# Optimization experiments

Measured on AMD Instinct MI355X. Metric: run time of the kernel, lower is better.

Reference implementation:

```python
import jax, jax.numpy as jnp
import numpy as np

B, T, H, W, C = 1, 16, 56, 56, 256
NH = 8
WS = (8, 7, 7)
SS = (4, 3, 3)
HID = 4 * C
N = WS[0] * WS[1] * WS[2]  # 392 tokens per window


def _rel_index(ws):
    wt, wh, ww = ws
    coords = np.stack(np.meshgrid(np.arange(wt), np.arange(wh), np.arange(ww), indexing='ij'))
    cf = coords.reshape(3, -1)
    rel = (cf[:, :, None] - cf[:, None, :]).transpose(1, 2, 0)
    rel[..., 0] += wt - 1
    rel[..., 1] += wh - 1
    rel[..., 2] += ww - 1
    rel[..., 0] *= (2 * wh - 1) * (2 * ww - 1)
    rel[..., 1] *= 2 * ww - 1
    return rel.sum(-1)  # (N, N) int


def _win_part_np(x, ws):
    b, t, h, w, c = x.shape
    x = x.reshape(b, t // ws[0], ws[0], h // ws[1], ws[1], w // ws[2], ws[2], c)
    return x.transpose(0, 1, 3, 5, 2, 4, 6, 7).reshape(-1, ws[0] * ws[1] * ws[2], c)


def _attn_mask(t, h, w, ws, ss):
    # static numpy construction of the shifted-window mask (nW, N, N)
    img = np.zeros((1, t, h, w, 1), dtype=np.float32)
    cnt = 0
    for d in (slice(-ws[0]), slice(-ws[0], -ss[0]), slice(-ss[0], None)):
        for hh in (slice(-ws[1]), slice(-ws[1], -ss[1]), slice(-ss[1], None)):
            for ww_ in (slice(-ws[2]), slice(-ws[2], -ss[2]), slice(-ss[2], None)):
                img[:, d, hh, ww_, :] = cnt
                cnt += 1
    mw = _win_part_np(img, ws).squeeze(-1)  # (nW, N)
    diff = mw[:, None, :] - mw[:, :, None]
    return np.where(diff != 0, np.float32(-100.0), np.float32(0.0))


_RPI = jnp.asarray(_rel_index(WS).reshape(-1))
_MASK = jnp.asarray(_attn_mask(T, H, W, WS, SS))  # (nW, N, N)


def _ln(x, g, b, eps=1e-5):
    mu = x.mean(-1, keepdims=True)
    var = ((x - mu) ** 2).mean(-1, keepdims=True)
    return (x - mu) * jax.lax.rsqrt(var + eps) * g + b


def _win_part(x, ws):
    b, t, h, w, c = x.shape
    x = x.reshape(b, t // ws[0], ws[0], h // ws[1], ws[1], w // ws[2], ws[2], c)
    return x.transpose(0, 1, 3, 5, 2, 4, 6, 7).reshape(-1, ws[0] * ws[1] * ws[2], c)


def _win_rev(win, ws, t, h, w):
    b = win.shape[0] // (t * h * w // (ws[0] * ws[1] * ws[2]))
    x = win.reshape(b, t // ws[0], h // ws[1], w // ws[2], ws[0], ws[1], ws[2], -1)
    return x.transpose(0, 1, 4, 2, 5, 3, 6, 7).reshape(b, t, h, w, -1)


def setup_inputs() -> dict:
    key = jax.random.key(0)
    ks = jax.random.split(key, 16)
    n_bias = (2 * WS[0] - 1) * (2 * WS[1] - 1) * (2 * WS[2] - 1)
    return {
        'x': jax.random.normal(ks[0], (B, T, H, W, C), jnp.float32),
        'norm1_g': jnp.ones((C,), jnp.float32),
        'norm1_b': jnp.zeros((C,), jnp.float32),
        'qkv_w': 0.02 * jax.random.normal(ks[1], (3 * C, C), jnp.float32),
        'qkv_b': jnp.zeros((3 * C,), jnp.float32),
        'rpb_table': 0.02 * jax.random.normal(ks[2], (n_bias, NH), jnp.float32),
        'proj_w': 0.02 * jax.random.normal(ks[3], (C, C), jnp.float32),
        'proj_b': jnp.zeros((C,), jnp.float32),
        'norm2_g': jnp.ones((C,), jnp.float32),
        'norm2_b': jnp.zeros((C,), jnp.float32),
        'fc1_w': 0.02 * jax.random.normal(ks[4], (HID, C), jnp.float32),
        'fc1_b': jnp.zeros((HID,), jnp.float32),
        'fc2_w': 0.02 * jax.random.normal(ks[5], (C, HID), jnp.float32),
        'fc2_b': jnp.zeros((C,), jnp.float32),
    }


def reference(x, norm1_g, norm1_b, qkv_w, qkv_b, rpb_table, proj_w, proj_b,
              norm2_g, norm2_b, fc1_w, fc1_b, fc2_w, fc2_b):
    hd = C // NH
    scale = hd ** -0.5
    shortcut = x
    h1 = _ln(x, norm1_g, norm1_b)
    # cyclic shift
    h1 = jnp.roll(h1, (-SS[0], -SS[1], -SS[2]), axis=(1, 2, 3))
    xw = _win_part(h1, WS)  # (B_, N, C)
    B_ = xw.shape[0]
    qkv = xw @ qkv_w.T + qkv_b  # (B_, N, 3C)
    qkv = qkv.reshape(B_, N, 3, NH, hd).transpose(2, 0, 3, 1, 4)
    q, k, v = qkv[0], qkv[1], qkv[2]  # (B_, NH, N, hd)
    attn = jnp.einsum('bhnd,bhmd->bhnm', q * scale, k)
    bias = rpb_table[_RPI].reshape(N, N, NH).transpose(2, 0, 1)  # (NH, N, N)
    attn = attn + bias[None]
    nW = _MASK.shape[0]
    attn = attn.reshape(B_ // nW, nW, NH, N, N) + _MASK[None, :, None]
    attn = jax.nn.softmax(attn, axis=-1).reshape(B_, NH, N, N)
    out = jnp.einsum('bhnm,bhmd->bhnd', attn, v).transpose(0, 2, 1, 3).reshape(B_, N, C)
    out = out @ proj_w.T + proj_b
    out = _win_rev(out, WS, T, H, W)
    out = jnp.roll(out, (SS[0], SS[1], SS[2]), axis=(1, 2, 3))
    x = shortcut + out
    # MLP with residual
    h2 = _ln(x, norm2_g, norm2_b)
    h2 = jax.nn.gelu(h2 @ fc1_w.T + fc1_b, approximate=False)
    return x + (h2 @ fc2_w.T + fc2_b)
```

## Files before the change

kernel.cpp:

```cpp
#include <hip/hip_runtime.h>
#include <hip/hip_bf16.h>
#include <cmath>

typedef unsigned short u16;
typedef unsigned int u32;

using bf16x8 = __attribute__((ext_vector_type(8))) short;
using f32x4  = __attribute__((ext_vector_type(4))) float;

__device__ __forceinline__ float b2f(u16 u) {
  union { u32 i; float f; } x; x.i = ((u32)u) << 16; return x.f;
}
__device__ __forceinline__ u16 f2b(float f) {
  union { float f; u32 i; } x; x.f = f;
  u32 r = x.i + 0x7fffu + ((x.i >> 16) & 1u);
  return (u16)(r >> 16);
}
__device__ __forceinline__ u32 cvtpk(float lo, float hi) {
  u32 r;
  asm("v_cvt_pk_bf16_f32 %0, %1, %2" : "=v"(r) : "v"(lo), "v"(hi));
  return r;
}
__device__ __forceinline__ float vexp2(float x) {
  float r;
  asm("v_exp_f32 %0, %1" : "=v"(r) : "v"(x));
  return r;
}
__device__ __forceinline__ void gload_lds16(const u16* g, u16* l) {
  __builtin_amdgcn_global_load_lds(
      (const __attribute__((address_space(1))) unsigned int*)g,
      (__attribute__((address_space(3))) unsigned int*)l, 16, 0, 0);
}

__global__ __launch_bounds__(256) void pre_k(
    const float* __restrict__ x, const float* __restrict__ n1g,
    const float* __restrict__ n1b, const float* __restrict__ qkvw,
    const float* __restrict__ projw, const float* __restrict__ fc1w,
    const float* __restrict__ fc2w, const float* __restrict__ rpb,
    u16* __restrict__ xw, u16* __restrict__ wts, u16* __restrict__ biasB) {
  const int blk = blockIdx.x;
  const int tid = threadIdx.x;
  if (blk < 12544) {
    const int wid = tid >> 6, lane = tid & 63;
    const int row = blk * 4 + wid;
    int widx = row / 392, n = row - widx * 392;
    int wt = widx >> 6, wh = (widx >> 3) & 7, ww = widx & 7;
    int ti = n / 49, rem = n - ti * 49, hi = rem / 7, wi = rem - hi * 7;
    int t = (wt * 8 + ti + 4) & 15;
    int h = wh * 7 + hi + 3; if (h >= 56) h -= 56;
    int w = ww * 7 + wi + 3; if (w >= 56) w -= 56;
    int srow = (t * 56 + h) * 56 + w;
    float4 v = *(const float4*)(x + (size_t)srow * 256 + lane * 4);
    float s = v.x + v.y + v.z + v.w;
    float sq = v.x * v.x + v.y * v.y + v.z * v.z + v.w * v.w;
    for (int o = 1; o < 64; o <<= 1) {
      s += __shfl_xor(s, o, 64);
      sq += __shfl_xor(sq, o, 64);
    }
    float mu = s * (1.0f / 256.0f);
    float rstd = rsqrtf(sq * (1.0f / 256.0f) - mu * mu + 1e-5f);
    float4 gg = *(const float4*)(n1g + lane * 4);
    float4 bb = *(const float4*)(n1b + lane * 4);
    ushort4 ov;
    ov.x = f2b((v.x - mu) * rstd * gg.x + bb.x);
    ov.y = f2b((v.y - mu) * rstd * gg.y + bb.y);
    ov.z = f2b((v.z - mu) * rstd * gg.z + bb.z);
    ov.w = f2b((v.w - mu) * rstd * gg.w + bb.w);
    *(ushort4*)(xw + (size_t)row * 256 + lane * 4) = ov;
  } else if (blk < 14144) {
    const int b = blk - 12544;
    const int sl = b / 25, qt = b - sl * 25;
    const int head = sl & 7, cls = sl >> 3;
    const int tb = (cls >> 2) & 1, hb = (cls >> 1) & 1, wb = cls & 1;
    const int lm = tid >> 4, kl = tid & 15;
    int q = qt * 16 + lm; if (q > 391) q = 391;
    const int ti = q / 49, rem = q - ti * 49, hi = rem / 7, wi = rem - hi * 7;
    const int cq = ti * 169 + hi * 13 + wi;
    const int rtq = tb ? (ti < 4 ? 1 : 2) : 0;
    const int rhq = hb ? (hi < 4 ? 1 : 2) : 0;
    const int rwq = wb ? (wi < 4 ? 1 : 2) : 0;
    const int labq = rtq * 9 + rhq * 3 + rwq;
    u16* ob = biasB + (size_t)b * 6400 + tid;
    for (int t = 0; t < 25; t++) {
      int k = t * 16 + kl;
      float v;
      if (k < 392) {
        int tk = k / 49, rk = k - tk * 49, hk = rk / 7, wk = rk - hk * 7;
        int ck = tk * 169 + hk * 13 + wk;
        float bv = rpb[(cq - ck + 1267) * 8 + head];
        int rt = tb ? (tk < 4 ? 1 : 2) : 0;
        int rh = hb ? (hk < 4 ? 1 : 2) : 0;
        int rw = wb ? (wk < 4 ? 1 : 2) : 0;
        if (rt * 9 + rh * 3 + rw != labq) bv -= 100.f;
        v = bv * 1.4426950408889634f;
      } else {
        v = -2081.f;
      }
      ob[t * 256] = f2b(v);
    }
  } else {
    int i = (blk - 14144) * 256 + tid;
    const float* src;
    int off;
    if (i < 196608)      { src = qkvw;  off = 0; }
    else if (i < 262144) { src = projw; off = 196608; }
    else if (i < 524288) { src = fc1w;  off = 262144; }
    else                 { src = fc2w;  off = 524288; }
    wts[i] = f2b(src[i - off]);
  }
}

__global__ __launch_bounds__(256) void ln_k(const float* __restrict__ src,
                                            const float* __restrict__ g,
                                            const float* __restrict__ b,
                                            u16* __restrict__ dst) {
  const int wid = threadIdx.x >> 6, lane = threadIdx.x & 63;
  const int row = blockIdx.x * 4 + wid;
  float4 v = *(const float4*)(src + (size_t)row * 256 + lane * 4);
  float s = v.x + v.y + v.z + v.w;
  float sq = v.x * v.x + v.y * v.y + v.z * v.z + v.w * v.w;
  for (int o = 1; o < 64; o <<= 1) {
    s += __shfl_xor(s, o, 64);
    sq += __shfl_xor(sq, o, 64);
  }
  float mu = s * (1.0f / 256.0f);
  float rstd = rsqrtf(sq * (1.0f / 256.0f) - mu * mu + 1e-5f);
  float4 gg = *(const float4*)(g + lane * 4);
  float4 bb = *(const float4*)(b + lane * 4);
  ushort4 ov;
  ov.x = f2b((v.x - mu) * rstd * gg.x + bb.x);
  ov.y = f2b((v.y - mu) * rstd * gg.y + bb.y);
  ov.z = f2b((v.z - mu) * rstd * gg.z + bb.z);
  ov.w = f2b((v.w - mu) * rstd * gg.w + bb.w);
  *(ushort4*)(dst + (size_t)row * 256 + lane * 4) = ov;
}

template <int EPI>
__global__ __launch_bounds__(512) void gemm_k(const u16* __restrict__ A,
                                              const u16* __restrict__ Bw,
                                              int K, int tilesN,
                                              const float* __restrict__ bias,
                                              u16* __restrict__ outb,
                                              float* __restrict__ outf,
                                              const float* __restrict__ res,
                                              float qscale) {
  __shared__ __align__(16) u16 As[2][256 * 32];
  __shared__ __align__(16) u16 Bs[2][128 * 32];
  const int tid = threadIdx.x;
  const int swzb = ((int)blockIdx.x & 7) * ((int)gridDim.x >> 3) +
                   ((int)blockIdx.x >> 3);
  const int tm = swzb / tilesN, tn = swzb - tm * tilesN;
  const int wid = tid >> 6, lane = tid & 63;
  const int wm = wid >> 1, wn = wid & 1;
  const int lm = lane & 15, lk = lane >> 4;
  f32x4 acc[4][4] = {};
  const u16* Ap = A + (size_t)tm * 256 * K;
  const u16* Bp = Bw + (size_t)tn * 128 * K;

  const int sA0 = wid * 128;
  const int sB0 = wid * 64;
  const int nt = K >> 5;

#define STAGE(bufi, kk)                                                       \
  {                                                                           \
    int S = sA0 + lane, r = S >> 2, cs = S & 3;                               \
    gload_lds16(Ap + (size_t)r * K + (kk) + ((cs ^ ((r >> 1) & 3)) << 3),     \
                &As[bufi][sA0 * 8]);                                          \
    S = sA0 + 64 + lane; r = S >> 2; cs = S & 3;                              \
    gload_lds16(Ap + (size_t)r * K + (kk) + ((cs ^ ((r >> 1) & 3)) << 3),     \
                &As[bufi][(sA0 + 64) * 8]);                                   \
    S = sB0 + lane; r = S >> 2; cs = S & 3;                                   \
    gload_lds16(Bp + (size_t)r * K + (kk) + ((cs ^ ((r >> 1) & 3)) << 3),     \
                &Bs[bufi][sB0 * 8]);                                          \
  }

  STAGE(0, 0);
  for (int t = 0; t < nt; t++) {
    const int cur = t & 1;
    if (t + 1 < nt) {
      STAGE(cur ^ 1, (t + 1) << 5);
      asm volatile("s_waitcnt vmcnt(3)" ::: "memory");
    } else {
      asm volatile("s_waitcnt vmcnt(0)" ::: "memory");
    }
    asm volatile("s_barrier" ::: "memory");
    __builtin_amdgcn_sched_barrier(0);
    bf16x8 af[4], bfr[4];
#pragma unroll
    for (int f = 0; f < 4; f++) {
      int ra = wm * 64 + f * 16 + lm;
      int rb = wn * 64 + f * 16 + lm;
      af[f] = *(const bf16x8*)((const char*)&As[cur][0] + ra * 64 +
                               ((lk ^ ((ra >> 1) & 3)) << 4));
      bfr[f] = *(const bf16x8*)((const char*)&Bs[cur][0] + rb * 64 +
                                ((lk ^ ((rb >> 1) & 3)) << 4));
    }
#pragma unroll
    for (int fm = 0; fm < 4; fm++)
#pragma unroll
      for (int fn = 0; fn < 4; fn++)
        acc[fm][fn] = __builtin_amdgcn_mfma_f32_16x16x32_bf16(
            af[fm], bfr[fn], acc[fm][fn], 0, 0, 0);
    asm volatile("s_barrier" ::: "memory");
  }
#undef STAGE

  const int rbase = tm * 256 + wm * 64, cbase = tn * 128 + wn * 64;
#pragma unroll
  for (int fm = 0; fm < 4; fm++) {
#pragma unroll
    for (int fn = 0; fn < 4; fn++) {
      const int col = cbase + fn * 16 + lm;
#pragma unroll
      for (int r = 0; r < 4; r++) {
        const int row = rbase + fm * 16 + lk * 4 + r;
        float v = acc[fm][fn][r] + bias[col];
        if (EPI == 0) {
          int s = col >> 8, rem = col & 255, head = rem >> 5, d = rem & 31;
          int widx = row / 392, n = row - widx * 392;
          size_t o;
          if (s == 2) {
            int c = n >> 5, gg2 = (n >> 3) & 3, e = n & 7;
            int lm2 = d & 15, half = d >> 4;
            o = 25690112u + (size_t)(widx * 8 + head) * 13312 +
                (size_t)(((c * 2 + half) * 64) + gg2 * 16 + lm2) * 8 + e;
          } else {
            if (s == 0) v *= qscale;
            o = (size_t)s * 12845056u +
                (((size_t)(widx * 8 + head)) * 392 + n) * 32 + d;
          }
          outb[o] = f2b(v);
        } else if (EPI == 1) {
          int widx = row / 392, n = row - widx * 392;
          int wt = widx >> 6, wh = (widx >> 3) & 7, ww = widx & 7;
          int ti = n / 49, rem2 = n - ti * 49, hi = rem2 / 7, wi = rem2 - hi * 7;
          int t = (wt * 8 + ti + 4) & 15;
          int h = wh * 7 + hi + 3; if (h >= 56) h -= 56;
          int w = ww * 7 + wi + 3; if (w >= 56) w -= 56;
          size_t dr = ((size_t)(t * 56 + h)) * 56 + w;
          outf[dr * 256 + col] = res[dr * 256 + col] + v;
        } else if (EPI == 2) {
          float gv = 0.5f * v * (1.0f + erff(v * 0.70710678f));
          outb[(size_t)row * 1024 + col] = f2b(gv);
        } else {
          outf[(size_t)row * 256 + col] = res[(size_t)row * 256 + col] + v;
        }
      }
    }
  }
}

__global__ __launch_bounds__(256) void attn_k(const u16* __restrict__ qg,
                                              const u16* __restrict__ kg,
                                              const u16* __restrict__ vfg,
                                              const u16* __restrict__ biasB,
                                              u16* __restrict__ attno) {
  __shared__ __align__(16) char lds[59904];
  const int bid = blockIdx.x;
  const int widx = bid >> 3;
  const int tid = threadIdx.x;
  const size_t base = (size_t)bid * 12544;
  const int tb = (widx >> 6) & 1;
  const int hb = (((widx >> 3) & 7) == 7) ? 1 : 0;
  const int wb = ((widx & 7) == 7) ? 1 : 0;
  const int sl = (tb * 4 + hb * 2 + wb) * 8 + (bid & 7);
  const int VOFF = 25088;
  const int POFF = 51712;

#pragma unroll
  for (int i = 0; i < 6; i++) {
    int s = i * 256 + tid, r = s >> 2, cs = s & 3;
    gload_lds16(kg + base + r * 32 + ((cs ^ ((r >> 1) & 3)) << 3),
                (u16*)(lds + (size_t)(i * 256 + (tid & ~63)) * 16));
  }
  if (tid < 32) {
    int s = 1536 + tid, r = s >> 2, cs = s & 3;
    gload_lds16(kg + base + r * 32 + ((cs ^ ((r >> 1) & 3)) << 3),
                (u16*)(lds + (size_t)1536 * 16));
  }
  {
    const u16* vsrc = vfg + (size_t)bid * 13312;
#pragma unroll
    for (int i = 0; i < 6; i++) {
      int s = i * 256 + tid;
      gload_lds16(vsrc + (size_t)s * 8,
                  (u16*)(lds + VOFF + (size_t)(i * 256 + (tid & ~63)) * 16));
    }
    if (tid < 128) {
      int s = 1536 + tid;
      gload_lds16(vsrc + (size_t)s * 8,
                  (u16*)(lds + VOFF + (size_t)(1536 + (tid & ~63)) * 16));
    }
  }
  __syncthreads();

  const int w = tid >> 6, lane = tid & 63;
  const int g = lane >> 4, lm = lane & 15;
  const int kswz = ((lm >> 1) & 3);
  char* PqW = lds + POFF + w * 2048 + lm * 128;
  const int swz = (lm & 7) << 4;
  const char* vlds = lds + VOFF + lane * 16;

  for (int qt = w; qt < 25; qt += 4) {
    const int q = qt * 16 + lm;
    const int qr = q < 391 ? q : 391;
    bf16x8 qf = *(const bf16x8*)(qg + base + (size_t)qr * 32 + g * 8);
    const u16* bp = biasB + ((size_t)(sl * 25 + qt) * 25) * 256 + lm * 16 + 4 * g;
    f32x4 st[25];
#pragma unroll
    for (int t = 0; t < 25; t++) {
      ushort4 bb = *(const ushort4*)(bp + t * 256);
      f32x4 bacc = {b2f(bb.x), b2f(bb.y), b2f(bb.z), b2f(bb.w)};
      int kr = (t < 24) ? (16 * t + lm) : (384 + (lm & 7));
      bf16x8 kf = *(const bf16x8*)(lds + kr * 64 + ((g ^ kswz) << 4));
      st[t] = __builtin_amdgcn_mfma_f32_16x16x32_bf16(kf, qf, bacc, 0, 0, 0);
    }
    float m = -3e38f;
#pragma unroll
    for (int t = 0; t < 25; t++)
      m = fmaxf(m, fmaxf(fmaxf(st[t][0], st[t][1]), fmaxf(st[t][2], st[t][3])));
    m = fmaxf(m, __shfl_xor(m, 16, 64));
    m = fmaxf(m, __shfl_xor(m, 32, 64));

    float sum = 0.f;
    f32x4 oa0 = {0.f, 0.f, 0.f, 0.f}, oa1 = {0.f, 0.f, 0.f, 0.f};
#pragma unroll
    for (int c = 0; c < 13; c++) {
      const int p64 = (c & 1) << 6;
      {
        int t = 2 * c;
        float e0 = vexp2(st[t][0] - m), e1 = vexp2(st[t][1] - m);
        float e2 = vexp2(st[t][2] - m), e3 = vexp2(st[t][3] - m);
        sum += (e0 + e1) + (e2 + e3);
        uint2 pp;
        pp.x = cvtpk(e0, e1);
        pp.y = cvtpk(e2, e3);
        *(uint2*)(PqW + ((p64 + 8 * g) ^ swz)) = pp;
      }
      {
        uint2 pp;
        if (c < 12) {
          int t = 2 * c + 1;
          float e0 = vexp2(st[t][0] - m), e1 = vexp2(st[t][1] - m);
          float e2 = vexp2(st[t][2] - m), e3 = vexp2(st[t][3] - m);
          sum += (e0 + e1) + (e2 + e3);
          pp.x = cvtpk(e0, e1);
          pp.y = cvtpk(e2, e3);
        } else {
          pp.x = 0u; pp.y = 0u;
        }
        *(uint2*)(PqW + ((p64 + 32 + 8 * g) ^ swz)) = pp;
      }
      bf16x8 pf = *(const bf16x8*)(PqW + ((p64 + 16 * g) ^ swz));
      const char* vp = vlds + c * 2048;
      bf16x8 v0 = *(const bf16x8*)vp;
      bf16x8 v1 = *(const bf16x8*)(vp + 1024);
      oa0 = __builtin_amdgcn_mfma_f32_16x16x32_bf16(pf, v0, oa0, 0, 0, 0);
      oa1 = __builtin_amdgcn_mfma_f32_16x16x32_bf16(pf, v1, oa1, 0, 0, 0);
    }
    sum += __shfl_xor(sum, 16, 64);
    sum += __shfl_xor(sum, 32, 64);
    const float inv = 1.f / sum;
#pragma unroll
    for (int r = 0; r < 4; r++) {
      int qq = qt * 16 + 4 * g + r;
      if (qq < 392) {
        u16* op = attno + ((size_t)(widx * 392 + qq)) * 256 + (bid & 7) * 32;
        op[lm] = f2b(oa0[r] * inv);
        op[16 + lm] = f2b(oa1[r] * inv);
      }
    }
  }
}

extern "C" void kernel_launch(void* const* d_in, const int* in_sizes, int n_in,
                              void* d_out, int out_size, void* d_ws,
                              size_t ws_size, hipStream_t stream) {
  const float* x     = (const float*)d_in[0];
  const float* n1g   = (const float*)d_in[1];
  const float* n1b   = (const float*)d_in[2];
  const float* qkvw  = (const float*)d_in[3];
  const float* qkvb  = (const float*)d_in[4];
  const float* rpb   = (const float*)d_in[5];
  const float* projw = (const float*)d_in[6];
  const float* projb = (const float*)d_in[7];
  const float* n2g   = (const float*)d_in[8];
  const float* n2b   = (const float*)d_in[9];
  const float* fc1w  = (const float*)d_in[10];
  const float* fc1b  = (const float*)d_in[11];
  const float* fc2w  = (const float*)d_in[12];
  const float* fc2b  = (const float*)d_in[13];

  const size_t NEED = 130547712;
  if (ws_size < NEED) return;

  char* ws = (char*)d_ws;
  u16* xw      = (u16*)(ws + 0LL);
  u16* qb      = (u16*)(ws + 25690112LL);
  u16* attno   = (u16*)(ws + 0LL);
  u16* h2      = (u16*)(ws + 0LL);
  u16* hid     = (u16*)(ws + 25690112LL);
  u16* biasB   = (u16*)(ws + 104333312LL);
  u16* wq      = (u16*)(ws + 128974848LL);
  u16* wp      = (u16*)(ws + 129368064LL);
  u16* w1      = (u16*)(ws + 129499136LL);
  u16* w2      = (u16*)(ws + 130023424LL);
  float* xres  = (float*)d_out;

  pre_k<<<17216, 256, 0, stream>>>(x, n1g, n1b, qkvw, projw, fc1w, fc2w, rpb,
                                   xw, wq, biasB);
  gemm_k<0><<<196 * 6, 512, 0, stream>>>(
      xw, wq, 256, 6, qkvb, qb, nullptr, nullptr,
      0.17677669529663687f * 1.4426950408889634f);
  attn_k<<<1024, 256, 0, stream>>>(qb, qb + 12845056, qb + 2 * 12845056, biasB,
                                   attno);
  gemm_k<1><<<196 * 2, 512, 0, stream>>>(attno, wp, 256, 2, projb, nullptr,
                                         xres, x, 0.f);
  ln_k<<<12544, 256, 0, stream>>>(xres, n2g, n2b, h2);
  gemm_k<2><<<196 * 8, 512, 0, stream>>>(h2, w1, 256, 8, fc1b, hid, nullptr,
                                         nullptr, 0.f);
  gemm_k<3><<<196 * 2, 512, 0, stream>>>(hid, w2, 1024, 2, fc2b, nullptr,
                                         (float*)d_out, xres, 0.f);
}
```

Baseline: 291.9 us.

## Fuse projection GEMM with residual and LayerNorm; use polynomial erf GELU

```diff
diff --git a/kernel.cpp b/kernel.cpp
--- a/kernel.cpp
+++ b/kernel.cpp
@@ -30,6 +30,18 @@
   __builtin_amdgcn_global_load_lds(
       (const __attribute__((address_space(1))) unsigned int*)g,
       (__attribute__((address_space(3))) unsigned int*)l, 16, 0, 0);
+}
+__device__ __forceinline__ float fast_gelu(float v) {
+  float u = 0.70710678118f * v;
+  float au = fabsf(u);
+  float t = 1.f / (1.f + 0.3275911f * au);
+  float p = t * (0.254829592f +
+            t * (-0.284496736f +
+            t * (1.421413741f + t * (-1.453152027f + t * 1.061405429f))));
+  float e = vexp2(-au * au * 1.4426950408889634f);
+  float erf_abs = 1.f - p * e;
+  float er = (v < 0.f) ? -erf_abs : erf_abs;
+  return 0.5f * v * (1.f + er);
 }
 
 __global__ __launch_bounds__(256) void pre_k(
@@ -110,31 +122,6 @@
   }
 }
 
-__global__ __launch_bounds__(256) void ln_k(const float* __restrict__ src,
-                                            const float* __restrict__ g,
-                                            const float* __restrict__ b,
-                                            u16* __restrict__ dst) {
-  const int wid = threadIdx.x >> 6, lane = threadIdx.x & 63;
-  const int row = blockIdx.x * 4 + wid;
-  float4 v = *(const float4*)(src + (size_t)row * 256 + lane * 4);
-  float s = v.x + v.y + v.z + v.w;
-  float sq = v.x * v.x + v.y * v.y + v.z * v.z + v.w * v.w;
-  for (int o = 1; o < 64; o <<= 1) {
-    s += __shfl_xor(s, o, 64);
-    sq += __shfl_xor(sq, o, 64);
-  }
-  float mu = s * (1.0f / 256.0f);
-  float rstd = rsqrtf(sq * (1.0f / 256.0f) - mu * mu + 1e-5f);
-  float4 gg = *(const float4*)(g + lane * 4);
-  float4 bb = *(const float4*)(b + lane * 4);
-  ushort4 ov;
-  ov.x = f2b((v.x - mu) * rstd * gg.x + bb.x);
-  ov.y = f2b((v.y - mu) * rstd * gg.y + bb.y);
-  ov.z = f2b((v.z - mu) * rstd * gg.z + bb.z);
-  ov.w = f2b((v.w - mu) * rstd * gg.w + bb.w);
-  *(ushort4*)(dst + (size_t)row * 256 + lane * 4) = ov;
-}
-
 template <int EPI>
 __global__ __launch_bounds__(512) void gemm_k(const u16* __restrict__ A,
                                               const u16* __restrict__ Bw,
@@ -230,23 +217,153 @@
                 (((size_t)(widx * 8 + head)) * 392 + n) * 32 + d;
           }
           outb[o] = f2b(v);
-        } else if (EPI == 1) {
-          int widx = row / 392, n = row - widx * 392;
-          int wt = widx >> 6, wh = (widx >> 3) & 7, ww = widx & 7;
-          int ti = n / 49, rem2 = n - ti * 49, hi = rem2 / 7, wi = rem2 - hi * 7;
-          int t = (wt * 8 + ti + 4) & 15;
-          int h = wh * 7 + hi + 3; if (h >= 56) h -= 56;
-          int w = ww * 7 + wi + 3; if (w >= 56) w -= 56;
-          size_t dr = ((size_t)(t * 56 + h)) * 56 + w;
-          outf[dr * 256 + col] = res[dr * 256 + col] + v;
         } else if (EPI == 2) {
-          float gv = 0.5f * v * (1.0f + erff(v * 0.70710678f));
-          outb[(size_t)row * 1024 + col] = f2b(gv);
+          outb[(size_t)row * 1024 + col] = f2b(fast_gelu(v));
         } else {
           outf[(size_t)row * 256 + col] = res[(size_t)row * 256 + col] + v;
         }
       }
     }
+  }
+}
+
+__global__ __launch_bounds__(512) void proj_ln_k(
+    const u16* __restrict__ A, const u16* __restrict__ Bw,
+    const float* __restrict__ pb, const float* __restrict__ x,
+    const float* __restrict__ n2g, const float* __restrict__ n2b,
+    float* __restrict__ xres, u16* __restrict__ h2) {
+  __shared__ __align__(16) u16 As[2][128 * 32];
+  __shared__ __align__(16) u16 Bs[2][256 * 32];
+  const int tid = threadIdx.x;
+  const int tm = ((int)blockIdx.x & 7) * ((int)gridDim.x >> 3) +
+                 ((int)blockIdx.x >> 3);
+  const int wid = tid >> 6, lane = tid & 63;
+  const int wm = wid >> 2, wn = wid & 3;
+  const int lm = lane & 15, lk = lane >> 4;
+  f32x4 acc[4][4] = {};
+  const u16* Ap = A + (size_t)tm * 128 * 256;
+
+#define PSTAGE(bufi, kk)                                                      \
+  {                                                                           \
+    int S = wid * 64 + lane, r = S >> 2, cs = S & 3;                          \
+    gload_lds16(A + (size_t)tm * 32768 + (size_t)r * 256 + (kk) +             \
+                    ((cs ^ ((r >> 1) & 3)) << 3),                             \
+                &As[bufi][(wid * 64) * 8]);                                   \
+    S = wid * 128 + lane; r = S >> 2; cs = S & 3;                             \
+    gload_lds16(Bw + (size_t)r * 256 + (kk) + ((cs ^ ((r >> 1) & 3)) << 3),   \
+                &Bs[bufi][(wid * 128) * 8]);                                  \
+    S = wid * 128 + 64 + lane; r = S >> 2; cs = S & 3;                        \
+    gload_lds16(Bw + (size_t)r * 256 + (kk) + ((cs ^ ((r >> 1) & 3)) << 3),   \
+                &Bs[bufi][(wid * 128 + 64) * 8]);                             \
+  }
+
+  PSTAGE(0, 0);
+  for (int t = 0; t < 8; t++) {
+    const int cur = t & 1;
+    if (t < 7) {
+      PSTAGE(cur ^ 1, (t + 1) << 5);
+      asm volatile("s_waitcnt vmcnt(3)" ::: "memory");
+    } else {
+      asm volatile("s_waitcnt vmcnt(0)" ::: "memory");
+    }
+    asm volatile("s_barrier" ::: "memory");
+    __builtin_amdgcn_sched_barrier(0);
+    bf16x8 af[4], bfr[4];
+#pragma unroll
+    for (int f = 0; f < 4; f++) {
+      int ra = wm * 64 + f * 16 + lm;
+      int rb = wn * 64 + f * 16 + lm;
+      af[f] = *(const bf16x8*)((const char*)&As[cur][0] + ra * 64 +
+                               ((lk ^ ((ra >> 1) & 3)) << 4));
+      bfr[f] = *(const bf16x8*)((const char*)&Bs[cur][0] + rb * 64 +
+                                ((lk ^ ((rb >> 1) & 3)) << 4));
+    }
+#pragma unroll
+    for (int fm = 0; fm < 4; fm++)
+#pragma unroll
+      for (int fn = 0; fn < 4; fn++)
+        acc[fm][fn] = __builtin_amdgcn_mfma_f32_16x16x32_bf16(
+            af[fm], bfr[fn], acc[fm][fn], 0, 0, 0);
+    asm volatile("s_barrier" ::: "memory");
+  }
+#undef PSTAGE
+  (void)Ap;
+
+  int dr_[4][4];
+#pragma unroll
+  for (int fm = 0; fm < 4; fm++) {
+#pragma unroll
+    for (int r = 0; r < 4; r++) {
+      int row = tm * 128 + wm * 64 + fm * 16 + lk * 4 + r;
+      int widx = row / 392, n = row - widx * 392;
+      int wt = widx >> 6, wh = (widx >> 3) & 7, ww = widx & 7;
+      int ti = n / 49, rem2 = n - ti * 49, hi = rem2 / 7, wi = rem2 - hi * 7;
+      int t = (wt * 8 + ti + 4) & 15;
+      int h = wh * 7 + hi + 3; if (h >= 56) h -= 56;
+      int w = ww * 7 + wi + 3; if (w >= 56) w -= 56;
+      dr_[fm][r] = (t * 56 + h) * 56 + w;
+    }
+  }
+#pragma unroll
+  for (int fn = 0; fn < 4; fn++) {
+    int col = wn * 64 + fn * 16 + lm;
+    float bv = pb[col];
+#pragma unroll
+    for (int fm = 0; fm < 4; fm++)
+#pragma unroll
+      for (int r = 0; r < 4; r++) {
+        size_t o = (size_t)dr_[fm][r] * 256 + col;
+        float r2 = x[o] + acc[fm][fn][r] + bv;
+        xres[o] = r2;
+        acc[fm][fn][r] = r2;
+      }
+  }
+  float* ps = (float*)&As[0][0];
+  float* qs = ps + 512;
+  float* mur = qs + 512;
+  float* rsr = mur + 128;
+#pragma unroll
+  for (int fm = 0; fm < 4; fm++)
+#pragma unroll
+    for (int r = 0; r < 4; r++) {
+      float s1 = 0.f, s2 = 0.f;
+#pragma unroll
+      for (int fn = 0; fn < 4; fn++) {
+        float v = acc[fm][fn][r];
+        s1 += v;
+        s2 += v * v;
+      }
+      s1 += __shfl_xor(s1, 1, 64); s2 += __shfl_xor(s2, 1, 64);
+      s1 += __shfl_xor(s1, 2, 64); s2 += __shfl_xor(s2, 2, 64);
+      s1 += __shfl_xor(s1, 4, 64); s2 += __shfl_xor(s2, 4, 64);
+      s1 += __shfl_xor(s1, 8, 64); s2 += __shfl_xor(s2, 8, 64);
+      if (lm == 0) {
+        int rr = wm * 64 + fm * 16 + lk * 4 + r;
+        ps[wn * 128 + rr] = s1;
+        qs[wn * 128 + rr] = s2;
+      }
+    }
+  __syncthreads();
+  if (tid < 128) {
+    float S = ps[tid] + ps[128 + tid] + ps[256 + tid] + ps[384 + tid];
+    float Q = qs[tid] + qs[128 + tid] + qs[256 + tid] + qs[384 + tid];
+    float mu = S * (1.f / 256.f);
+    mur[tid] = mu;
+    rsr[tid] = rsqrtf(Q * (1.f / 256.f) - mu * mu + 1e-5f);
+  }
+  __syncthreads();
+#pragma unroll
+  for (int fn = 0; fn < 4; fn++) {
+    int col = wn * 64 + fn * 16 + lm;
+    float gv = n2g[col], bbv = n2b[col];
+#pragma unroll
+    for (int fm = 0; fm < 4; fm++)
+#pragma unroll
+      for (int r = 0; r < 4; r++) {
+        int rr = wm * 64 + fm * 16 + lk * 4 + r;
+        h2[(size_t)dr_[fm][r] * 256 + col] =
+            f2b((acc[fm][fn][r] - mur[rr]) * rsr[rr] * gv + bbv);
+      }
   }
 }
 
@@ -398,8 +515,8 @@
   u16* xw      = (u16*)(ws + 0LL);
   u16* qb      = (u16*)(ws + 25690112LL);
   u16* attno   = (u16*)(ws + 0LL);
-  u16* h2      = (u16*)(ws + 0LL);
-  u16* hid     = (u16*)(ws + 25690112LL);
+  u16* hid     = (u16*)(ws + 0LL);
+  u16* h2      = (u16*)(ws + 102760448LL);
   u16* biasB   = (u16*)(ws + 104333312LL);
   u16* wq      = (u16*)(ws + 128974848LL);
   u16* wp      = (u16*)(ws + 129368064LL);
@@ -414,9 +531,7 @@
       0.17677669529663687f * 1.4426950408889634f);
   attn_k<<<1024, 256, 0, stream>>>(qb, qb + 12845056, qb + 2 * 12845056, biasB,
                                    attno);
-  gemm_k<1><<<196 * 2, 512, 0, stream>>>(attno, wp, 256, 2, projb, nullptr,
-                                         xres, x, 0.f);
-  ln_k<<<12544, 256, 0, stream>>>(xres, n2g, n2b, h2);
+  proj_ln_k<<<392, 512, 0, stream>>>(attno, wp, projb, x, n2g, n2b, xres, h2);
   gemm_k<2><<<196 * 8, 512, 0, stream>>>(h2, w1, 256, 8, fc1b, hid, nullptr,
                                          nullptr, 0.f);
   gemm_k<3><<<196 * 2, 512, 0, stream>>>(hid, w2, 1024, 2, fc2b, nullptr,
```

Result: slower. 310.0 us (+6.2%).
